# Performance work log

Hardware: AMD Instinct MI355X
Metric: run time of the kernel (lower is better)

Reference implementation:

```python
import jax, jax.numpy as jnp
import numpy as np

N = 50000; E = 800000; F_IN = 128; H = 16; G = 256
DIMS = [F_IN, H, 2 * H, 4 * H, 4 * H, 8 * H]
EPS = 1e-5


def setup_inputs() -> dict:
    key = jax.random.key(0)
    ks = iter(jax.random.split(key, 40))
    inp = {}
    inp["x"] = jax.random.normal(next(ks), (N, F_IN), dtype=jnp.float32)
    inp["edge_index"] = jax.random.randint(next(ks), (2, E), 0, N, dtype=jnp.int32)
    inp["edge_weight"] = jax.random.uniform(next(ks), (E,), dtype=jnp.float32)
    inp["batch"] = jnp.sort(jax.random.randint(next(ks), (N,), 0, G, dtype=jnp.int32))
    for i in range(5):
        din, dout = DIMS[i], DIMS[i + 1]
        inp[f"W{i+1}"] = jax.random.normal(next(ks), (din, dout), dtype=jnp.float32) / np.sqrt(din).astype(np.float32)
        inp[f"b{i+1}"] = jnp.zeros((dout,), jnp.float32)
        inp[f"g{i+1}"] = jnp.ones((dout,), jnp.float32)
        inp[f"bt{i+1}"] = jnp.zeros((dout,), jnp.float32)
    inp["fc1_w"] = jax.random.normal(next(ks), (8 * H, 4 * H), dtype=jnp.float32) / np.sqrt(8 * H).astype(np.float32)
    inp["fc1_b"] = jnp.zeros((4 * H,), jnp.float32)
    inp["fc2_w"] = jax.random.normal(next(ks), (4 * H, 1), dtype=jnp.float32) / np.sqrt(4 * H).astype(np.float32)
    inp["fc2_b"] = jnp.zeros((1,), jnp.float32)
    return inp


def _gcn_norm(edge_index, edge_weight, n):
    # PyG GCNConv: add self-loops (weight 1), symmetric deg^-1/2 normalization.
    loop = jnp.arange(n, dtype=edge_index.dtype)
    row = jnp.concatenate([edge_index[0], loop])  # source
    col = jnp.concatenate([edge_index[1], loop])  # target
    w = jnp.concatenate([edge_weight, jnp.ones((n,), edge_weight.dtype)])
    deg = jax.ops.segment_sum(w, col, num_segments=n)
    dis = jnp.where(deg > 0, jax.lax.rsqrt(jnp.maximum(deg, 1e-12)), 0.0)
    return row, col, dis[row] * w * dis[col]


def _bn(h, g, b):
    # BatchNorm1d, training-mode batch statistics (biased variance, eps=1e-5)
    mu = h.mean(0)
    v = h.var(0)
    return g * (h - mu) * jax.lax.rsqrt(v + EPS) + b


def reference(x, edge_index, edge_weight, batch,
              W1, b1, g1, bt1, W2, b2, g2, bt2, W3, b3, g3, bt3,
              W4, b4, g4, bt4, W5, b5, g5, bt5,
              fc1_w, fc1_b, fc2_w, fc2_b):
    n = x.shape[0]
    row, col, norm = _gcn_norm(edge_index, edge_weight, n)

    def conv(h, W, b):
        m = h @ W                                   # [N, dout] dense transform
        agg = jax.ops.segment_sum(m[row] * norm[:, None], col, num_segments=n)
        return agg + b

    h = _bn(jax.nn.relu(conv(x, W1, b1)), g1, bt1)
    h = _bn(jax.nn.relu(conv(h, W2, b2)), g2, bt2)
    h = _bn(jax.nn.relu(conv(h, W3, b3)), g3, bt3)
    h = jax.nn.relu(_bn(conv(h, W4, b4), g4, bt4))   # layer4: conv->bn->relu
    h = _bn(conv(h, W5, b5), g5, bt5)                # layer5: conv->bn
    pooled = jax.ops.segment_sum(h, batch, num_segments=G)  # global_add_pool -> [G, 8H]
    p = jax.nn.relu(pooled)
    p = jax.nn.relu(p @ fc1_w + fc1_b)
    # dropout is identity in eval mode
    return (p @ fc2_w + fc2_b).reshape(-1)          # [G]
```

## Files before the change

### kernel.cpp

```cpp
#include <hip/hip_runtime.h>
#include <stdint.h>

#define NN 50000
#define NE 800000
#define NG 256
#define NBUCKET 16
#define PARTSZ (NBUCKET * 256)

#define NBKT 391
#define ABLK 391
#define ASLICE 2048
#define BCAP 2560

__device__ __forceinline__ float bf2f(unsigned short u) {
    return __uint_as_float(((unsigned)u) << 16);
}
__device__ __forceinline__ unsigned short f2bf(float f) {
    unsigned b = __float_as_uint(f);
    return (unsigned short)((b + 0x7FFF + ((b >> 16) & 1)) >> 16);
}

__global__ void kA1(const int* __restrict__ col, int* __restrict__ bb, float* part, int e) {
    __shared__ int cnt[NBKT];
    for (int j = threadIdx.x; j < NBKT; j += 256) cnt[j] = 0;
    for (int i = blockIdx.x * 256 + threadIdx.x; i < 5 * PARTSZ; i += ABLK * 256) part[i] = 0.f;
    __syncthreads();
    int start = blockIdx.x * ASLICE;
    int end = min(start + ASLICE, e);
    for (int i = start + threadIdx.x; i < end; i += 256)
        atomicAdd(&cnt[col[i] >> 7], 1);
    __syncthreads();
    for (int j = threadIdx.x; j < NBKT; j += 256) bb[blockIdx.x * NBKT + j] = cnt[j];
}

__global__ void kA2a(int* __restrict__ bb, int* __restrict__ totals) {
    __shared__ int v[ABLK];
    int k = blockIdx.x;
    for (int b = threadIdx.x; b < ABLK; b += 256) v[b] = bb[b * NBKT + k];
    __syncthreads();
    if (threadIdx.x == 0) {
        int run = 0;
        for (int b = 0; b < ABLK; ++b) { int t = v[b]; v[b] = run; run += t; }
        totals[k] = run;
    }
    __syncthreads();
    for (int b = threadIdx.x; b < ABLK; b += 256) bb[b * NBKT + k] = v[b];
}

__global__ void kA2b(const int* __restrict__ totals, int* __restrict__ bucketbase) {
    __shared__ int v[NBKT];
    for (int j = threadIdx.x; j < NBKT; j += 256) v[j] = totals[j];
    __syncthreads();
    if (threadIdx.x == 0) {
        int run = 0;
        for (int k = 0; k < NBKT; ++k) { int t = v[k]; v[k] = run; run += t; }
        bucketbase[NBKT] = run;
    }
    __syncthreads();
    for (int j = threadIdx.x; j < NBKT; j += 256) bucketbase[j] = v[j];
}

__global__ void kA3g(const int* __restrict__ row, const int* __restrict__ col,
                     const float* __restrict__ ew, const int* __restrict__ bb,
                     const int* __restrict__ bucketbase, int2* __restrict__ staging,
                     const float* __restrict__ x, const float* __restrict__ W0,
                     float* __restrict__ m1, int e, int n) {
    __shared__ int cur[NBKT];
    __shared__ float Wl[128 * 16];
    int tid = threadIdx.x;
    if ((int)blockIdx.x < ABLK) {
        for (int j = tid; j < NBKT; j += 256)
            cur[j] = bucketbase[j] + bb[blockIdx.x * NBKT + j];
        __syncthreads();
        int start = blockIdx.x * ASLICE;
        int end = min(start + ASLICE, e);
        for (int i = start + tid; i < end; i += 256) {
            int c = col[i];
            int p = atomicAdd(&cur[c >> 7], 1);
            staging[p] = make_int2(row[i] | ((c & 127) << 16), __float_as_int(ew[i]));
        }
        return;
    }
    int bid = (int)blockIdx.x - ABLK;
    for (int i = tid; i < 128 * 16 / 4; i += 256)
        ((float4*)Wl)[i] = ((const float4*)W0)[i];
    __syncthreads();
    int jq = tid % 4, group = tid / 4;
    int node0 = (bid * 64 + group) * 2;
    const float4* h4 = (const float4*)x;
    int hb[2]; bool val[2];
#pragma unroll
    for (int i = 0; i < 2; ++i) {
        int nd = node0 + i;
        val[i] = nd < n;
        hb[i] = (val[i] ? nd : n - 1) * 32;
    }
    float4 acc[2];
    acc[0] = {0,0,0,0}; acc[1] = {0,0,0,0};
#pragma unroll 4
    for (int k4 = 0; k4 < 32; ++k4) {
        const float* wb = &Wl[(k4 * 4) * 16 + jq * 4];
        float4 w0 = *(const float4*)(wb);
        float4 w1 = *(const float4*)(wb + 16);
        float4 w2 = *(const float4*)(wb + 32);
        float4 w3 = *(const float4*)(wb + 48);
#pragma unroll
        for (int i = 0; i < 2; ++i) {
            float4 hv = h4[hb[i] + k4];
            acc[i].x += hv.x*w0.x + hv.y*w1.x + hv.z*w2.x + hv.w*w3.x;
            acc[i].y += hv.x*w0.y + hv.y*w1.y + hv.z*w2.y + hv.w*w3.y;
            acc[i].z += hv.x*w0.z + hv.y*w1.z + hv.z*w2.z + hv.w*w3.z;
            acc[i].w += hv.x*w0.w + hv.y*w1.w + hv.z*w2.w + hv.w*w3.w;
        }
    }
#pragma unroll
    for (int i = 0; i < 2; ++i)
        if (val[i]) ((float4*)m1)[(node0 + i) * 4 + jq] = acc[i];
}

__global__ void __launch_bounds__(256) kB(const int* __restrict__ bucketbase,
                                          const int2* __restrict__ staging,
                                          int2* __restrict__ csr, int* __restrict__ ptr,
                                          float* __restrict__ dis, int n) {
    __shared__ int2 st[BCAP];
    __shared__ int2 outb[BCAP];
    __shared__ int hist[129];
    __shared__ int cur[128];
    int k = blockIdx.x, t = threadIdx.x;
    int base = bucketbase[k], cnt = bucketbase[k + 1] - base;
    int node0 = k << 7;
    int ncov = min(128, n - node0);
    if (t < 129) hist[t] = 0;
    __syncthreads();
    if (cnt <= BCAP) {
        for (int i = t; i < cnt; i += 256) {
            int2 v = staging[base + i];
            st[i] = v;
            atomicAdd(&hist[v.x >> 16], 1);
        }
        __syncthreads();
        if (t == 0) {
            int run = 0;
            for (int j = 0; j < 128; ++j) { int h = hist[j]; hist[j] = run; run += h; }
            hist[128] = run;
        }
        __syncthreads();
        if (t < 128) cur[t] = hist[t];
        if (t < ncov) ptr[node0 + t] = base + hist[t];
        __syncthreads();
        for (int i = t; i < cnt; i += 256) {
            int2 v = st[i];
            int j = v.x >> 16;
            int p = atomicAdd(&cur[j], 1);
            outb[p] = make_int2(v.x & 0xFFFF, v.y);
        }
        __syncthreads();
        for (int i = t; i < cnt; i += 256) csr[base + i] = outb[i];
        if (t < ncov) {
            float s = 1.f;
            int a = hist[t], b2 = hist[t + 1];
            for (int p = a; p < b2; ++p) s += __int_as_float(outb[p].y);
            dis[node0 + t] = rsqrtf(s);
        }
    } else {
        for (int i = t; i < cnt; i += 256) atomicAdd(&hist[staging[base + i].x >> 16], 1);
        __syncthreads();
        if (t == 0) {
            int run = 0;
            for (int j = 0; j < 128; ++j) { int h = hist[j]; hist[j] = run; run += h; }
            hist[128] = run;
        }
        __syncthreads();
        if (t < 128) cur[t] = hist[t];
        if (t < ncov) ptr[node0 + t] = base + hist[t];
        __syncthreads();
        for (int i = t; i < cnt; i += 256) {
            int2 v = staging[base + i];
            int j = v.x >> 16;
            int p = atomicAdd(&cur[j], 1);
            csr[base + p] = make_int2(v.x & 0xFFFF, v.y);
        }
        __threadfence_block();
        __syncthreads();
        if (t < ncov) {
            float s = 1.f;
            int a = hist[t], b2 = hist[t + 1];
            for (int p = a; p < b2; ++p) s += __int_as_float(csr[base + p].y);
            dis[node0 + t] = rsqrtf(s);
        }
    }
    if (k == gridDim.x - 1 && t == 0) ptr[n] = bucketbase[NBKT];
}

__global__ void k_l1gather(const float* __restrict__ src, const int* __restrict__ ptr,
                           int2* __restrict__ csr, const float* __restrict__ dis,
                           const float* __restrict__ bias, float* __restrict__ partOut,
                           float* __restrict__ out, int n) {
    __shared__ float ls[16], lq[16];
    int tid = threadIdx.x;
    if (tid < 16) { ls[tid] = 0.f; lq[tid] = 0.f; }
    __syncthreads();
    int t = blockIdx.x * 256 + tid;
    int node = t >> 2;
    int l4 = t & 3;
    bool valid = node < n;
    int nc = valid ? node : n - 1;
    const float4* s4 = (const float4*)src;
    float dc = dis[nc];
    float w0 = dc * dc;
    float4 v = s4[nc * 4 + l4];
    float4 acc = { w0 * v.x, w0 * v.y, w0 * v.z, w0 * v.w };
    int p0 = ptr[nc], p1 = ptr[nc + 1];
    int p = p0;
    for (; p + 4 <= p1; p += 4) {
        int2 c0 = csr[p], c1 = csr[p+1], c2 = csr[p+2], c3 = csr[p+3];
        float e0 = dis[c0.x] * __int_as_float(c0.y) * dc;
        float e1 = dis[c1.x] * __int_as_float(c1.y) * dc;
        float e2 = dis[c2.x] * __int_as_float(c2.y) * dc;
        float e3 = dis[c3.x] * __int_as_float(c3.y) * dc;
        float4 u0 = s4[c0.x * 4 + l4];
        float4 u1 = s4[c1.x * 4 + l4];
        float4 u2 = s4[c2.x * 4 + l4];
        float4 u3 = s4[c3.x * 4 + l4];
        acc.x += e0*u0.x + e1*u1.x + e2*u2.x + e3*u3.x;
        acc.y += e0*u0.y + e1*u1.y + e2*u2.y + e3*u3.y;
        acc.z += e0*u0.z + e1*u1.z + e2*u2.z + e3*u3.z;
        acc.w += e0*u0.w + e1*u1.w + e2*u2.w + e3*u3.w;
        if (l4 == 0) {
            csr[p]   = make_int2(c0.x, __float_as_int(e0));
            csr[p+1] = make_int2(c1.x, __float_as_int(e1));
            csr[p+2] = make_int2(c2.x, __float_as_int(e2));
            csr[p+3] = make_int2(c3.x, __float_as_int(e3));
        }
    }
    for (; p < p1; ++p) {
        int2 ce = csr[p];
        float w = dis[ce.x] * __int_as_float(ce.y) * dc;
        float4 u = s4[ce.x * 4 + l4];
        acc.x += w*u.x; acc.y += w*u.y; acc.z += w*u.z; acc.w += w*u.w;
        if (l4 == 0) csr[p] = make_int2(ce.x, __float_as_int(w));
    }
    float4 b = ((const float4*)bias)[l4];
    acc.x = fmaxf(acc.x + b.x, 0.f);
    acc.y = fmaxf(acc.y + b.y, 0.f);
    acc.z = fmaxf(acc.z + b.z, 0.f);
    acc.w = fmaxf(acc.w + b.w, 0.f);
    if (valid) ((float4*)out)[nc * 4 + l4] = acc;
    float s0 = valid ? acc.x : 0.f, s1 = valid ? acc.y : 0.f;
    float s2 = valid ? acc.z : 0.f, s3 = valid ? acc.w : 0.f;
    float q0 = s0*s0, q1 = s1*s1, q2 = s2*s2, q3 = s3*s3;
    for (int off = 4; off < 64; off <<= 1) {
        s0 += __shfl_down(s0, off, 64); s1 += __shfl_down(s1, off, 64);
        s2 += __shfl_down(s2, off, 64); s3 += __shfl_down(s3, off, 64);
        q0 += __shfl_down(q0, off, 64); q1 += __shfl_down(q1, off, 64);
        q2 += __shfl_down(q2, off, 64); q3 += __shfl_down(q3, off, 64);
    }
    int lane = tid & 63;
    if (lane < 4) {
        atomicAdd(&ls[4*lane+0], s0); atomicAdd(&ls[4*lane+1], s1);
        atomicAdd(&ls[4*lane+2], s2); atomicAdd(&ls[4*lane+3], s3);
        atomicAdd(&lq[4*lane+0], q0); atomicAdd(&lq[4*lane+1], q1);
        atomicAdd(&lq[4*lane+2], q2); atomicAdd(&lq[4*lane+3], q3);
    }
    __syncthreads();
    int bkt = (blockIdx.x & (NBUCKET - 1)) * 256;
    if (tid < 16) {
        atomicAdd(&partOut[bkt + tid], ls[tid]);
        atomicAdd(&partOut[bkt + 128 + tid], lq[tid]);
    }
}

template <int D, int BF16>
__device__ __forceinline__ float4 load_row(const void* src, int node, int l4) {
    if (BF16) {
        const unsigned short* sb = (const unsigned short*)src;
        ushort4 r = *(const ushort4*)(sb + (size_t)node * D + (l4 << 2));
        float4 f;
        f.x = bf2f(r.x); f.y = bf2f(r.y); f.z = bf2f(r.z); f.w = bf2f(r.w);
        return f;
    } else {
        const float4* s4 = (const float4*)src;
        return s4[(size_t)node * (D / 4) + l4];
    }
}

template <int DIN, int DOUT, int EP, int POSTAFF, int PREAFF, int RELU,
          int BF16IN, int BF16OUT, int NPB>
__global__ void __launch_bounds__(256) k_fused(
        const void* __restrict__ src, const int* __restrict__ ptr,
        const int2* __restrict__ csr, const float* __restrict__ dis,
        const float* __restrict__ partIn, const float* __restrict__ gmv,
        const float* __restrict__ btv, const float* __restrict__ W,
        const float* __restrict__ bias, float* __restrict__ partOut,
        void* __restrict__ out, int n) {
    const int TPN1 = DIN / 4, LPN = TPN1 * EP, GN1 = 256 / LPN;
    const int TPN2 = DOUT / 4, G2 = 256 / TPN2;
    const int HS = DIN + 4;
    __shared__ float Wl[DIN * DOUT];
    __shared__ float hrow[NPB * HS];
    __shared__ float scs[DIN], shs[DIN];
    __shared__ float ls[DOUT], lq[DOUT];
    int tid = threadIdx.x;
    for (int i = tid; i < DIN * DOUT / 4; i += 256)
        ((float4*)Wl)[i] = ((const float4*)W)[i];
    if (tid < DIN) {
        float s = 0.f, q = 0.f;
#pragma unroll
        for (int b2 = 0; b2 < NBUCKET; ++b2) {
            s += partIn[b2 * 256 + tid];
            q += partIn[b2 * 256 + 128 + tid];
        }
        float mu = s / (float)n;
        float var = q / (float)n - mu * mu;
        float a = gmv[tid] * rsqrtf(var + 1e-5f);
        scs[tid] = a;
        shs[tid] = btv[tid] - mu * a;
    }
    if (tid < DOUT) { ls[tid] = 0.f; lq[tid] = 0.f; }
    __syncthreads();

    int nodebase = blockIdx.x * NPB;
    {
        int grp = tid / LPN, r = tid % LPN;
        int e0 = r / TPN1, l4 = r % TPN1;
        float4 sc = ((const float4*)scs)[l4];
        float4 sh = ((const float4*)shs)[l4];
#pragma unroll
        for (int pass = 0; pass < NPB / GN1; ++pass) {
            int nl = pass * GN1 + grp;
            int node = nodebase + nl;
            int nc = node < n ? node : n - 1;
            float4 acc = {0.f, 0.f, 0.f, 0.f};
            float sumw = 0.f;
            if (e0 == 0) {
                float d = dis[nc];
                float w0 = d * d;
                float4 v = load_row<DIN, BF16IN>(src, nc, l4);
                if (PREAFF) {
                    v.x = fmaxf(sc.x*v.x+sh.x, 0.f); v.y = fmaxf(sc.y*v.y+sh.y, 0.f);
                    v.z = fmaxf(sc.z*v.z+sh.z, 0.f); v.w = fmaxf(sc.w*v.w+sh.w, 0.f);
                }
                acc.x = w0*v.x; acc.y = w0*v.y; acc.z = w0*v.z; acc.w = w0*v.w;
                sumw = w0;
            }
            int p0 = ptr[nc], p1 = ptr[nc + 1];
            int p = p0 + e0;
            for (; p + 3 * EP < p1; p += 4 * EP) {
                int2 c0 = csr[p], c1 = csr[p + EP], c2 = csr[p + 2*EP], c3 = csr[p + 3*EP];
                float e0w = __int_as_float(c0.y), e1w = __int_as_float(c1.y);
                float e2w = __int_as_float(c2.y), e3w = __int_as_float(c3.y);
                float4 u0 = load_row<DIN, BF16IN>(src, c0.x, l4);
                float4 u1 = load_row<DIN, BF16IN>(src, c1.x, l4);
                float4 u2 = load_row<DIN, BF16IN>(src, c2.x, l4);
                float4 u3 = load_row<DIN, BF16IN>(src, c3.x, l4);
                if (PREAFF) {
                    u0.x = fmaxf(sc.x*u0.x+sh.x,0.f); u0.y = fmaxf(sc.y*u0.y+sh.y,0.f);
                    u0.z = fmaxf(sc.z*u0.z+sh.z,0.f); u0.w = fmaxf(sc.w*u0.w+sh.w,0.f);
                    u1.x = fmaxf(sc.x*u1.x+sh.x,0.f); u1.y = fmaxf(sc.y*u1.y+sh.y,0.f);
                    u1.z = fmaxf(sc.z*u1.z+sh.z,0.f); u1.w = fmaxf(sc.w*u1.w+sh.w,0.f);
                    u2.x = fmaxf(sc.x*u2.x+sh.x,0.f); u2.y = fmaxf(sc.y*u2.y+sh.y,0.f);
                    u2.z = fmaxf(sc.z*u2.z+sh.z,0.f); u2.w = fmaxf(sc.w*u2.w+sh.w,0.f);
                    u3.x = fmaxf(sc.x*u3.x+sh.x,0.f); u3.y = fmaxf(sc.y*u3.y+sh.y,0.f);
                    u3.z = fmaxf(sc.z*u3.z+sh.z,0.f); u3.w = fmaxf(sc.w*u3.w+sh.w,0.f);
                }
                acc.x += e0w*u0.x + e1w*u1.x + e2w*u2.x + e3w*u3.x;
                acc.y += e0w*u0.y + e1w*u1.y + e2w*u2.y + e3w*u3.y;
                acc.z += e0w*u0.z + e1w*u1.z + e2w*u2.z + e3w*u3.z;
                acc.w += e0w*u0.w + e1w*u1.w + e2w*u2.w + e3w*u3.w;
                if (POSTAFF) sumw += e0w + e1w + e2w + e3w;
            }
            for (; p < p1; p += EP) {
                int2 ce = csr[p];
                float w = __int_as_float(ce.y);
                float4 u = load_row<DIN, BF16IN>(src, ce.x, l4);
                if (PREAFF) {
                    u.x = fmaxf(sc.x*u.x+sh.x,0.f); u.y = fmaxf(sc.y*u.y+sh.y,0.f);
                    u.z = fmaxf(sc.z*u.z+sh.z,0.f); u.w = fmaxf(sc.w*u.w+sh.w,0.f);
                }
                acc.x += w*u.x; acc.y += w*u.y; acc.z += w*u.z; acc.w += w*u.w;
                if (POSTAFF) sumw += w;
            }
#pragma unroll
            for (int off = TPN1; off < LPN; off <<= 1) {
                acc.x += __shfl_xor(acc.x, off, 64);
                acc.y += __shfl_xor(acc.y, off, 64);
                acc.z += __shfl_xor(acc.z, off, 64);
                acc.w += __shfl_xor(acc.w, off, 64);
                if (POSTAFF) sumw += __shfl_xor(sumw, off, 64);
            }
            if (POSTAFF) {
                acc.x = sc.x * acc.x + sh.x * sumw;
                acc.y = sc.y * acc.y + sh.y * sumw;
                acc.z = sc.z * acc.z + sh.z * sumw;
                acc.w = sc.w * acc.w + sh.w * sumw;
            }
            if (e0 == 0) *(float4*)&hrow[nl * HS + (l4 << 2)] = acc;
        }
    }
    __syncthreads();
    {
        int jq = tid % TPN2, g2 = tid / TPN2;
        float4 bv = ((const float4*)bias)[jq];
        float4 sv = {0,0,0,0}, qv = {0,0,0,0};
        for (int nl = g2; nl < NPB; nl += G2) {
            int node = nodebase + nl;
            bool valid = node < n;
            float4 a = {0.f, 0.f, 0.f, 0.f};
#pragma unroll
            for (int k4 = 0; k4 < DIN / 4; ++k4) {
                float4 hv = *(const float4*)&hrow[nl * HS + (k4 << 2)];
                const float* wb = &Wl[(k4 * 4) * DOUT + jq * 4];
                float4 w0 = *(const float4*)(wb);
                float4 w1 = *(const float4*)(wb + DOUT);
                float4 w2 = *(const float4*)(wb + 2 * DOUT);
                float4 w3 = *(const float4*)(wb + 3 * DOUT);
                a.x += hv.x*w0.x + hv.y*w1.x + hv.z*w2.x + hv.w*w3.x;
                a.y += hv.x*w0.y + hv.y*w1.y + hv.z*w2.y + hv.w*w3.y;
                a.z += hv.x*w0.z + hv.y*w1.z + hv.z*w2.z + hv.w*w3.z;
                a.w += hv.x*w0.w + hv.y*w1.w + hv.z*w2.w + hv.w*w3.w;
            }
            a.x += bv.x; a.y += bv.y; a.z += bv.z; a.w += bv.w;
            if (RELU) {
                a.x = fmaxf(a.x, 0.f); a.y = fmaxf(a.y, 0.f);
                a.z = fmaxf(a.z, 0.f); a.w = fmaxf(a.w, 0.f);
            }
            if (valid) {
                if (BF16OUT) {
                    ushort4 o;
                    o.x = f2bf(a.x); o.y = f2bf(a.y); o.z = f2bf(a.z); o.w = f2bf(a.w);
                    *(ushort4*)((unsigned short*)out + (size_t)node * DOUT + (jq << 2)) = o;
                } else {
                    ((float4*)out)[(size_t)node * TPN2 + jq] = a;
                }
                sv.x += a.x; sv.y += a.y; sv.z += a.z; sv.w += a.w;
                qv.x += a.x*a.x; qv.y += a.y*a.y; qv.z += a.z*a.z; qv.w += a.w*a.w;
            }
        }
        for (int off = TPN2; off < 64; off <<= 1) {
            sv.x += __shfl_down(sv.x, off, 64); sv.y += __shfl_down(sv.y, off, 64);
            sv.z += __shfl_down(sv.z, off, 64); sv.w += __shfl_down(sv.w, off, 64);
            qv.x += __shfl_down(qv.x, off, 64); qv.y += __shfl_down(qv.y, off, 64);
            qv.z += __shfl_down(qv.z, off, 64); qv.w += __shfl_down(qv.w, off, 64);
        }
        int lane = tid & 63;
        if (lane < TPN2) {
            atomicAdd(&ls[4*lane+0], sv.x); atomicAdd(&ls[4*lane+1], sv.y);
            atomicAdd(&ls[4*lane+2], sv.z); atomicAdd(&ls[4*lane+3], sv.w);
            atomicAdd(&lq[4*lane+0], qv.x); atomicAdd(&lq[4*lane+1], qv.y);
            atomicAdd(&lq[4*lane+2], qv.z); atomicAdd(&lq[4*lane+3], qv.w);
        }
        __syncthreads();
        int bkt = (blockIdx.x & (NBUCKET - 1)) * 256;
        if (tid < DOUT) {
            atomicAdd(&partOut[bkt + tid], ls[tid]);
            atomicAdd(&partOut[bkt + 128 + tid], lq[tid]);
        }
    }
}

template <int POSTAFF, int PREAFF>
__global__ void k_sgather(const unsigned short* __restrict__ src, const int* __restrict__ ptr,
                          const int2* __restrict__ csr, const float* __restrict__ dis,
                          const float* __restrict__ partIn, const float* __restrict__ gmv,
                          const float* __restrict__ btv, float* __restrict__ out, int n) {
    const int TPN = 16, EP = 4, LPN = 64;
    __shared__ float scs[64], shs[64];
    int tid = threadIdx.x;
    if (tid < 64) {
        float s = 0.f, q = 0.f;
#pragma unroll
        for (int b2 = 0; b2 < NBUCKET; ++b2) {
            s += partIn[b2 * 256 + tid];
            q += partIn[b2 * 256 + 128 + tid];
        }
        float mu = s / (float)n;
        float var = q / (float)n - mu * mu;
        float a = gmv[tid] * rsqrtf(var + 1e-5f);
        scs[tid] = a;
        shs[tid] = btv[tid] - mu * a;
    }
    __syncthreads();
    int t = blockIdx.x * 256 + tid;
    int node = t / LPN;
    int r = t - node * LPN;
    int e0 = r / TPN;
    int l4 = r - e0 * TPN;
    bool valid = node < n;
    int nc = valid ? node : n - 1;
    float4 sc = ((const float4*)scs)[l4];
    float4 sh = ((const float4*)shs)[l4];
    float4 acc = {0.f, 0.f, 0.f, 0.f};
    float sumw = 0.f;
    if (e0 == 0) {
        float d = dis[nc];
        float w0 = d * d;
        float4 v = load_row<64, 1>(src, nc, l4);
        if (PREAFF) {
            v.x = fmaxf(sc.x*v.x+sh.x, 0.f); v.y = fmaxf(sc.y*v.y+sh.y, 0.f);
            v.z = fmaxf(sc.z*v.z+sh.z, 0.f); v.w = fmaxf(sc.w*v.w+sh.w, 0.f);
        }
        acc.x = w0*v.x; acc.y = w0*v.y; acc.z = w0*v.z; acc.w = w0*v.w;
        sumw = w0;
    }
    int p0 = ptr[nc], p1 = ptr[nc + 1];
    int p = p0 + e0;
    for (; p + 3 * EP < p1; p += 4 * EP) {
        int2 c0 = csr[p], c1 = csr[p + EP], c2 = csr[p + 2*EP], c3 = csr[p + 3*EP];
        float e0w = __int_as_float(c0.y), e1w = __int_as_float(c1.y);
        float e2w = __int_as_float(c2.y), e3w = __int_as_float(c3.y);
        float4 u0 = load_row<64, 1>(src, c0.x, l4);
        float4 u1 = load_row<64, 1>(src, c1.x, l4);
        float4 u2 = load_row<64, 1>(src, c2.x, l4);
        float4 u3 = load_row<64, 1>(src, c3.x, l4);
        if (PREAFF) {
            u0.x = fmaxf(sc.x*u0.x+sh.x,0.f); u0.y = fmaxf(sc.y*u0.y+sh.y,0.f);
            u0.z = fmaxf(sc.z*u0.z+sh.z,0.f); u0.w = fmaxf(sc.w*u0.w+sh.w,0.f);
            u1.x = fmaxf(sc.x*u1.x+sh.x,0.f); u1.y = fmaxf(sc.y*u1.y+sh.y,0.f);
            u1.z = fmaxf(sc.z*u1.z+sh.z,0.f); u1.w = fmaxf(sc.w*u1.w+sh.w,0.f);
            u2.x = fmaxf(sc.x*u2.x+sh.x,0.f); u2.y = fmaxf(sc.y*u2.y+sh.y,0.f);
            u2.z = fmaxf(sc.z*u2.z+sh.z,0.f); u2.w = fmaxf(sc.w*u2.w+sh.w,0.f);
            u3.x = fmaxf(sc.x*u3.x+sh.x,0.f); u3.y = fmaxf(sc.y*u3.y+sh.y,0.f);
            u3.z = fmaxf(sc.z*u3.z+sh.z,0.f); u3.w = fmaxf(sc.w*u3.w+sh.w,0.f);
        }
        acc.x += e0w*u0.x + e1w*u1.x + e2w*u2.x + e3w*u3.x;
        acc.y += e0w*u0.y + e1w*u1.y + e2w*u2.y + e3w*u3.y;
        acc.z += e0w*u0.z + e1w*u1.z + e2w*u2.z + e3w*u3.z;
        acc.w += e0w*u0.w + e1w*u1.w + e2w*u2.w + e3w*u3.w;
        if (POSTAFF) sumw += e0w + e1w + e2w + e3w;
    }
    for (; p < p1; p += EP) {
        int2 ce = csr[p];
        float w = __int_as_float(ce.y);
        float4 u = load_row<64, 1>(src, ce.x, l4);
        if (PREAFF) {
            u.x = fmaxf(sc.x*u.x+sh.x,0.f); u.y = fmaxf(sc.y*u.y+sh.y,0.f);
            u.z = fmaxf(sc.z*u.z+sh.z,0.f); u.w = fmaxf(sc.w*u.w+sh.w,0.f);
        }
        acc.x += w*u.x; acc.y += w*u.y; acc.z += w*u.z; acc.w += w*u.w;
        if (POSTAFF) sumw += w;
    }
#pragma unroll
    for (int off = TPN; off < LPN; off <<= 1) {
        acc.x += __shfl_xor(acc.x, off, 64);
        acc.y += __shfl_xor(acc.y, off, 64);
        acc.z += __shfl_xor(acc.z, off, 64);
        acc.w += __shfl_xor(acc.w, off, 64);
        if (POSTAFF) sumw += __shfl_xor(sumw, off, 64);
    }
    if (POSTAFF) {
        acc.x = sc.x * acc.x + sh.x * sumw;
        acc.y = sc.y * acc.y + sh.y * sumw;
        acc.z = sc.z * acc.z + sh.z * sumw;
        acc.w = sc.w * acc.w + sh.w * sumw;
    }
    if (valid && e0 == 0) ((float4*)out)[nc * TPN + l4] = acc;
}

template <int DOUT, int RELU, int BF16OUT>
__global__ void k_sgemm(const float* __restrict__ h, const float* __restrict__ W,
                        const float* __restrict__ bias, float* __restrict__ partOut,
                        void* __restrict__ m, int n) {
    const int TPN = DOUT / 4, GPB = 256 / TPN, NPT = 4;
    __shared__ float Wl[64 * DOUT];
    __shared__ float ls[DOUT], lq[DOUT];
    int tid = threadIdx.x;
    for (int i = tid; i < 64 * DOUT / 4; i += 256)
        ((float4*)Wl)[i] = ((const float4*)W)[i];
    if (tid < DOUT) { ls[tid] = 0.f; lq[tid] = 0.f; }
    __syncthreads();

    int jq = tid % TPN;
    int group = tid / TPN;
    int node0 = (blockIdx.x * GPB + group) * NPT;
    const float4* h4 = (const float4*)h;
    int hb[NPT]; bool val[NPT];
#pragma unroll
    for (int i = 0; i < NPT; ++i) {
        int nd = node0 + i;
        val[i] = nd < n;
        hb[i] = (val[i] ? nd : n - 1) * 16;
    }
    float4 acc[NPT];
#pragma unroll
    for (int i = 0; i < NPT; ++i) acc[i] = {0.f, 0.f, 0.f, 0.f};
#pragma unroll 4
    for (int k4 = 0; k4 < 16; ++k4) {
        const float* wb = &Wl[(k4 * 4) * DOUT + jq * 4];
        float4 w0 = *(const float4*)(wb);
        float4 w1 = *(const float4*)(wb + DOUT);
        float4 w2 = *(const float4*)(wb + 2 * DOUT);
        float4 w3 = *(const float4*)(wb + 3 * DOUT);
#pragma unroll
        for (int i = 0; i < NPT; ++i) {
            float4 hv = h4[hb[i] + k4];
            acc[i].x += hv.x*w0.x + hv.y*w1.x + hv.z*w2.x + hv.w*w3.x;
            acc[i].y += hv.x*w0.y + hv.y*w1.y + hv.z*w2.y + hv.w*w3.y;
            acc[i].z += hv.x*w0.z + hv.y*w1.z + hv.z*w2.z + hv.w*w3.z;
            acc[i].w += hv.x*w0.w + hv.y*w1.w + hv.z*w2.w + hv.w*w3.w;
        }
    }
    float4 bv = ((const float4*)bias)[jq];
    float4 sv = {0,0,0,0}, qv = {0,0,0,0};
#pragma unroll
    for (int i = 0; i < NPT; ++i) {
        float4 a = acc[i];
        a.x += bv.x; a.y += bv.y; a.z += bv.z; a.w += bv.w;
        if (RELU) {
            a.x = fmaxf(a.x, 0.f); a.y = fmaxf(a.y, 0.f);
            a.z = fmaxf(a.z, 0.f); a.w = fmaxf(a.w, 0.f);
        }
        if (val[i]) {
            if (BF16OUT) {
                ushort4 o;
                o.x = f2bf(a.x); o.y = f2bf(a.y); o.z = f2bf(a.z); o.w = f2bf(a.w);
                *(ushort4*)((unsigned short*)m + (size_t)(node0 + i) * DOUT + (jq << 2)) = o;
            } else {
                ((float4*)m)[(size_t)(node0 + i) * TPN + jq] = a;
            }
            sv.x += a.x; sv.y += a.y; sv.z += a.z; sv.w += a.w;
            qv.x += a.x*a.x; qv.y += a.y*a.y; qv.z += a.z*a.z; qv.w += a.w*a.w;
        }
    }
    for (int off = TPN; off < 64; off <<= 1) {
        sv.x += __shfl_down(sv.x, off, 64); sv.y += __shfl_down(sv.y, off, 64);
        sv.z += __shfl_down(sv.z, off, 64); sv.w += __shfl_down(sv.w, off, 64);
        qv.x += __shfl_down(qv.x, off, 64); qv.y += __shfl_down(qv.y, off, 64);
        qv.z += __shfl_down(qv.z, off, 64); qv.w += __shfl_down(qv.w, off, 64);
    }
    int lane = tid & 63;
    if (lane < TPN) {
        atomicAdd(&ls[4*lane+0], sv.x); atomicAdd(&ls[4*lane+1], sv.y);
        atomicAdd(&ls[4*lane+2], sv.z); atomicAdd(&ls[4*lane+3], sv.w);
        atomicAdd(&lq[4*lane+0], qv.x); atomicAdd(&lq[4*lane+1], qv.y);
        atomicAdd(&lq[4*lane+2], qv.z); atomicAdd(&lq[4*lane+3], qv.w);
    }
    __syncthreads();
    int bkt = (blockIdx.x & (NBUCKET - 1)) * 256;
    if (tid < DOUT) {
        atomicAdd(&partOut[bkt + tid], ls[tid]);
        atomicAdd(&partOut[bkt + 128 + tid], lq[tid]);
    }
}

__global__ void k_poolhead(const float* __restrict__ h, const int* __restrict__ batch,
                           const float* __restrict__ partIn, const float* __restrict__ gmv,
                           const float* __restrict__ btv,
                           const float* __restrict__ fc1w, const float* __restrict__ fc1b,
                           const float* __restrict__ fc2w, const float* __restrict__ fc2b,
                           float* __restrict__ out, int n) {
    __shared__ float tmp[256];
    __shared__ float pl[128];
    __shared__ float scs[128], shs[128];
    int g = blockIdx.x;
    int tid = threadIdx.x;
    if (tid < 128) {
        float s = 0.f, q = 0.f;
#pragma unroll
        for (int b2 = 0; b2 < NBUCKET; ++b2) {
            s += partIn[b2 * 256 + tid];
            q += partIn[b2 * 256 + 128 + tid];
        }
        float mu = s / (float)n;
        float var = q / (float)n - mu * mu;
        float a = gmv[tid] * rsqrtf(var + 1e-5f);
        scs[tid] = a;
        shs[tid] = btv[tid] - mu * a;
    }
    int j = tid & 127, prt = tid >> 7;
    int a = 0, b = n;
    while (a < b) { int mid = (a + b) >> 1; if (batch[mid] < g) a = mid + 1; else b = mid; }
    int lo = a;
    b = n;
    while (a < b) { int mid = (a + b) >> 1; if (batch[mid] < g + 1) a = mid + 1; else b = mid; }
    int hi = a;

    float acc = 0.f;
    for (int node = lo + prt; node < hi; node += 2) acc += h[(long)node * 128 + j];
    tmp[tid] = acc;
    __syncthreads();
    if (tid < 128) {
        float cnt = (float)(hi - lo);
        float p = scs[tid] * (tmp[tid] + tmp[tid + 128]) + shs[tid] * cnt;
        pl[tid] = fmaxf(p, 0.f);
    }
    __syncthreads();
    if (tid < 64) {
        float v1 = fc1b[tid];
        for (int k = 0; k < 128; ++k) v1 += pl[k] * fc1w[k * 64 + tid];
        v1 = fmaxf(v1, 0.f);
        float v = v1 * fc2w[tid];
        for (int off = 32; off > 0; off >>= 1) v += __shfl_down(v, off, 64);
        if (tid == 0) out[g] = v + fc2b[0];
    }
}

extern "C" void kernel_launch(void* const* d_in, const int* in_sizes, int n_in,
                              void* d_out, int out_size, void* d_ws, size_t ws_size,
                              hipStream_t stream) {
    const float* x     = (const float*)d_in[0];
    const int*   ei    = (const int*)d_in[1];
    const float* ew    = (const float*)d_in[2];
    const int*   batch = (const int*)d_in[3];
    const float *W[5], *b[5], *gm[5], *bt[5];
    for (int i = 0; i < 5; ++i) {
        W[i]  = (const float*)d_in[4 + 4 * i];
        b[i]  = (const float*)d_in[5 + 4 * i];
        gm[i] = (const float*)d_in[6 + 4 * i];
        bt[i] = (const float*)d_in[7 + 4 * i];
    }
    const float* fc1w = (const float*)d_in[24];
    const float* fc1b = (const float*)d_in[25];
    const float* fc2w = (const float*)d_in[26];
    const float* fc2b = (const float*)d_in[27];
    float* out = (float*)d_out;

    char* wsb = (char*)d_ws;
    float* dis    = (float*)wsb;  wsb += sizeof(float) * NN;
    int*   ptr    = (int*)wsb;    wsb += sizeof(int) * (NN + 4);
    int*   bb     = (int*)wsb;    wsb += sizeof(int) * ABLK * NBKT;
    int*   totals = (int*)wsb;    wsb += sizeof(int) * (NBKT + 1);
    int*   bbase  = (int*)wsb;    wsb += sizeof(int) * (NBKT + 3);
    wsb = (char*)(((uintptr_t)wsb + 15) & ~(uintptr_t)15);
    int2*  staging= (int2*)wsb;   wsb += sizeof(int2) * NE;
    int2*  csr    = (int2*)wsb;   wsb += sizeof(int2) * NE;
    float* part   = (float*)wsb;  wsb += sizeof(float) * 5 * PARTSZ;
    unsigned short* bufB1 = (unsigned short*)wsb;  wsb += sizeof(unsigned short) * (size_t)NN * 64;
    unsigned short* bufB2 = (unsigned short*)wsb;  wsb += sizeof(unsigned short) * (size_t)NN * 64;
    float* buf1   = (float*)wsb;  wsb += sizeof(float) * (size_t)NN * 64;
    float* buf2   = (float*)wsb;  wsb += sizeof(float) * (size_t)NN * 128;

    const int* row = ei;
    const int* col = ei + NE;
    const int B = 256;
    const int NBF = (NN + 15) / 16;
    const int GB1 = (NN + 127) / 128;

    kA1<<<ABLK, B, 0, stream>>>(col, bb, part, NE);
    kA2a<<<NBKT, B, 0, stream>>>(bb, totals);
    kA2b<<<1, B, 0, stream>>>(totals, bbase);
    kA3g<<<ABLK + GB1, B, 0, stream>>>(row, col, ew, bb, bbase, staging, x, W[0], buf1, NE, NN);
    kB<<<NBKT, B, 0, stream>>>(bbase, staging, csr, ptr, dis, NN);

    k_l1gather<<<(NN * 4 + 255) / 256, B, 0, stream>>>(buf1, ptr, csr, dis,
                                                       b[0], part + 0 * PARTSZ, buf2, NN);

    k_fused<16, 32, 4, 1, 0, 1, 0, 1, 16><<<NBF, B, 0, stream>>>(
        buf2, ptr, csr, dis, part + 0 * PARTSZ, gm[0], bt[0],
        W[1], b[1], part + 1 * PARTSZ, bufB1, NN);
    k_fused<32, 64, 4, 1, 0, 1, 1, 1, 16><<<NBF, B, 0, stream>>>(
        bufB1, ptr, csr, dis, part + 1 * PARTSZ, gm[1], bt[1],
        W[2], b[2], part + 2 * PARTSZ, bufB2, NN);

    k_sgather<1, 0><<<(int)(((long)NN * 64 + 255) / 256), B, 0, stream>>>(
        bufB2, ptr, csr, dis, part + 2 * PARTSZ, gm[2], bt[2], buf1, NN);
    k_sgemm<64, 0, 1><<<(NN + 63) / 64, B, 0, stream>>>(buf1, W[3], b[3], part + 3 * PARTSZ, bufB1, NN);

    k_sgather<0, 1><<<(int)(((long)NN * 64 + 255) / 256), B, 0, stream>>>(
        bufB1, ptr, csr, dis, part + 3 * PARTSZ, gm[3], bt[3], buf1, NN);
    k_sgemm<128, 0, 0><<<(NN + 31) / 32, B, 0, stream>>>(buf1, W[4], b[4], part + 4 * PARTSZ, buf2, NN);

    k_poolhead<<<NG, B, 0, stream>>>(buf2, batch, part + 4 * PARTSZ, gm[4], bt[4],
                                     fc1w, fc1b, fc2w, fc2b, out, NN);
}
```

Measured before the change: 406.8 us.

## Split layer-3 conv into aggregate-then-transform gather and GEMM kernels

```diff
diff --git a/kernel.cpp b/kernel.cpp
--- a/kernel.cpp
+++ b/kernel.cpp
@@ -458,15 +458,15 @@
     }
 }
 
-template <int POSTAFF, int PREAFF>
+template <int D, int POSTAFF, int PREAFF>
 __global__ void k_sgather(const unsigned short* __restrict__ src, const int* __restrict__ ptr,
                           const int2* __restrict__ csr, const float* __restrict__ dis,
                           const float* __restrict__ partIn, const float* __restrict__ gmv,
                           const float* __restrict__ btv, float* __restrict__ out, int n) {
-    const int TPN = 16, EP = 4, LPN = 64;
-    __shared__ float scs[64], shs[64];
+    const int TPN = D / 4, EP = 4, LPN = TPN * EP;
+    __shared__ float scs[D], shs[D];
     int tid = threadIdx.x;
-    if (tid < 64) {
+    if (tid < D) {
         float s = 0.f, q = 0.f;
 #pragma unroll
         for (int b2 = 0; b2 < NBUCKET; ++b2) {
@@ -494,7 +494,7 @@
     if (e0 == 0) {
         float d = dis[nc];
         float w0 = d * d;
-        float4 v = load_row<64, 1>(src, nc, l4);
+        float4 v = load_row<D, 1>(src, nc, l4);
         if (PREAFF) {
             v.x = fmaxf(sc.x*v.x+sh.x, 0.f); v.y = fmaxf(sc.y*v.y+sh.y, 0.f);
             v.z = fmaxf(sc.z*v.z+sh.z, 0.f); v.w = fmaxf(sc.w*v.w+sh.w, 0.f);
@@ -508,10 +508,10 @@
         int2 c0 = csr[p], c1 = csr[p + EP], c2 = csr[p + 2*EP], c3 = csr[p + 3*EP];
         float e0w = __int_as_float(c0.y), e1w = __int_as_float(c1.y);
         float e2w = __int_as_float(c2.y), e3w = __int_as_float(c3.y);
-        float4 u0 = load_row<64, 1>(src, c0.x, l4);
-        float4 u1 = load_row<64, 1>(src, c1.x, l4);
-        float4 u2 = load_row<64, 1>(src, c2.x, l4);
-        float4 u3 = load_row<64, 1>(src, c3.x, l4);
+        float4 u0 = load_row<D, 1>(src, c0.x, l4);
+        float4 u1 = load_row<D, 1>(src, c1.x, l4);
+        float4 u2 = load_row<D, 1>(src, c2.x, l4);
+        float4 u3 = load_row<D, 1>(src, c3.x, l4);
         if (PREAFF) {
             u0.x = fmaxf(sc.x*u0.x+sh.x,0.f); u0.y = fmaxf(sc.y*u0.y+sh.y,0.f);
             u0.z = fmaxf(sc.z*u0.z+sh.z,0.f); u0.w = fmaxf(sc.w*u0.w+sh.w,0.f);
@@ -531,7 +531,7 @@
     for (; p < p1; p += EP) {
         int2 ce = csr[p];
         float w = __int_as_float(ce.y);
-        float4 u = load_row<64, 1>(src, ce.x, l4);
+        float4 u = load_row<D, 1>(src, ce.x, l4);
         if (PREAFF) {
             u.x = fmaxf(sc.x*u.x+sh.x,0.f); u.y = fmaxf(sc.y*u.y+sh.y,0.f);
             u.z = fmaxf(sc.z*u.z+sh.z,0.f); u.w = fmaxf(sc.w*u.w+sh.w,0.f);
@@ -556,15 +556,15 @@
     if (valid && e0 == 0) ((float4*)out)[nc * TPN + l4] = acc;
 }
 
-template <int DOUT, int RELU, int BF16OUT>
+template <int DIN, int DOUT, int RELU, int BF16OUT>
 __global__ void k_sgemm(const float* __restrict__ h, const float* __restrict__ W,
                         const float* __restrict__ bias, float* __restrict__ partOut,
                         void* __restrict__ m, int n) {
     const int TPN = DOUT / 4, GPB = 256 / TPN, NPT = 4;
-    __shared__ float Wl[64 * DOUT];
+    __shared__ float Wl[DIN * DOUT];
     __shared__ float ls[DOUT], lq[DOUT];
     int tid = threadIdx.x;
-    for (int i = tid; i < 64 * DOUT / 4; i += 256)
+    for (int i = tid; i < DIN * DOUT / 4; i += 256)
         ((float4*)Wl)[i] = ((const float4*)W)[i];
     if (tid < DOUT) { ls[tid] = 0.f; lq[tid] = 0.f; }
     __syncthreads();
@@ -578,13 +578,13 @@
     for (int i = 0; i < NPT; ++i) {
         int nd = node0 + i;
         val[i] = nd < n;
-        hb[i] = (val[i] ? nd : n - 1) * 16;
+        hb[i] = (val[i] ? nd : n - 1) * (DIN / 4);
     }
     float4 acc[NPT];
 #pragma unroll
     for (int i = 0; i < NPT; ++i) acc[i] = {0.f, 0.f, 0.f, 0.f};
 #pragma unroll 4
-    for (int k4 = 0; k4 < 16; ++k4) {
+    for (int k4 = 0; k4 < DIN / 4; ++k4) {
         const float* wb = &Wl[(k4 * 4) * DOUT + jq * 4];
         float4 w0 = *(const float4*)(wb);
         float4 w1 = *(const float4*)(wb + DOUT);
@@ -747,17 +747,18 @@
     k_fused<16, 32, 4, 1, 0, 1, 0, 1, 16><<<NBF, B, 0, stream>>>(
         buf2, ptr, csr, dis, part + 0 * PARTSZ, gm[0], bt[0],
         W[1], b[1], part + 1 * PARTSZ, bufB1, NN);
-    k_fused<32, 64, 4, 1, 0, 1, 1, 1, 16><<<NBF, B, 0, stream>>>(
-        bufB1, ptr, csr, dis, part + 1 * PARTSZ, gm[1], bt[1],
-        W[2], b[2], part + 2 * PARTSZ, bufB2, NN);
-
-    k_sgather<1, 0><<<(int)(((long)NN * 64 + 255) / 256), B, 0, stream>>>(
+
+    k_sgather<32, 1, 0><<<(int)(((long)NN * 32 + 255) / 256), B, 0, stream>>>(
+        bufB1, ptr, csr, dis, part + 1 * PARTSZ, gm[1], bt[1], buf1, NN);
+    k_sgemm<32, 64, 1, 1><<<(NN + 63) / 64, B, 0, stream>>>(buf1, W[2], b[2], part + 2 * PARTSZ, bufB2, NN);
+
+    k_sgather<64, 1, 0><<<(int)(((long)NN * 64 + 255) / 256), B, 0, stream>>>(
         bufB2, ptr, csr, dis, part + 2 * PARTSZ, gm[2], bt[2], buf1, NN);
-    k_sgemm<64, 0, 1><<<(NN + 63) / 64, B, 0, stream>>>(buf1, W[3], b[3], part + 3 * PARTSZ, bufB1, NN);
-
-    k_sgather<0, 1><<<(int)(((long)NN * 64 + 255) / 256), B, 0, stream>>>(
+    k_sgemm<64, 64, 0, 1><<<(NN + 63) / 64, B, 0, stream>>>(buf1, W[3], b[3], part + 3 * PARTSZ, bufB1, NN);
+
+    k_sgather<64, 0, 1><<<(int)(((long)NN * 64 + 255) / 256), B, 0, stream>>>(
         bufB1, ptr, csr, dis, part + 3 * PARTSZ, gm[3], bt[3], buf1, NN);
-    k_sgemm<128, 0, 0><<<(NN + 31) / 32, B, 0, stream>>>(buf1, W[4], b[4], part + 4 * PARTSZ, buf2, NN);
+    k_sgemm<64, 128, 0, 0><<<(NN + 31) / 32, B, 0, stream>>>(buf1, W[4], b[4], part + 4 * PARTSZ, buf2, NN);
 
     k_poolhead<<<NG, B, 0, stream>>>(buf2, batch, part + 4 * PARTSZ, gm[4], bt[4],
                                      fc1w, fc1b, fc2w, fc2b, out, NN);
```

Measured after the change: 396.5 us. 1.03x faster.
